# Kernel tuning notes

Hardware: AMD Instinct MI355X
Metric: run time of the kernel (lower is better)

The kernel has to match this reference:

```python
import jax, jax.numpy as jnp
import numpy as np

N, P, C = 100000, 64, 128
DIST_TH = 0.1


def setup_inputs() -> dict:
    key = jax.random.key(0)
    ks = jax.random.split(key, 12)
    xyz = jax.random.uniform(ks[0], (N, 3), jnp.float32) * 10.0  # room coords in [0,10)^3
    feature = jax.random.normal(ks[1], (N, C), jnp.float32)
    center = jax.random.uniform(ks[2], (P, 3), jnp.float32) * 10.0
    normal = jax.random.normal(ks[3], (P, 3), jnp.float32)
    normal = normal / jnp.linalg.norm(normal, axis=1, keepdims=True)
    pmin = center - 1.5  # axis-aligned extent used on axes 0,1
    pmax = center + 1.5
    inp = {
        'feature': feature, 'xyz': xyz,
        'plane_center': center, 'plane_normal': normal,
        'plane_min': pmin, 'plane_max': pmax,
        'W1': jax.random.normal(ks[4], (C, 2 * C), jnp.float32) * (1.0 / np.sqrt(C)),
        's1': jnp.ones((2 * C,), jnp.float32), 'b1': jnp.zeros((2 * C,), jnp.float32),
        'W2': jax.random.normal(ks[5], (2 * C, C), jnp.float32) * (1.0 / np.sqrt(2 * C)),
        's2': jnp.ones((C,), jnp.float32), 'b2': jnp.zeros((C,), jnp.float32),
        'W3': jax.random.normal(ks[6], (C, 1), jnp.float32) * (1.0 / np.sqrt(C)),
        'b3': jnp.zeros((1,), jnp.float32),
        'Wa': jax.random.normal(ks[7], (C, C), jnp.float32) * (1.0 / np.sqrt(C)),
        'Wm': jax.random.normal(ks[8], (C, C), jnp.float32) * (1.0 / np.sqrt(C)),
        'bm': jnp.zeros((C,), jnp.float32),
    }
    return inp


def reference(feature, xyz, plane_center, plane_normal, plane_min, plane_max,
              W1, s1, b1, W2, s2, b2, W3, b3, Wa, Wm, bm):
    # pointwise MLP (shared across planes): fc1 (conv+BN+ReLU), fc2 (conv+BN+ReLU)
    h = jax.nn.relu((feature @ W1) * s1 + b1)          # [N, 2C]
    h2 = jax.nn.relu((h @ W2) * s2 + b2)               # [N, C] == plane_feature
    logit = (h2 @ W3 + b3)[:, 0]                        # [N] fc3 logits (plane_result)

    # per-plane point membership masks (dense [N, P])
    proj = xyz @ plane_normal.T                         # [N, P]
    offs = jnp.sum(plane_center * plane_normal, axis=1) # [P]
    dist_mask = jnp.abs(proj - offs[None, :]) < DIST_TH
    rng = ((xyz[:, None, 0] >= plane_min[None, :, 0]) & (xyz[:, None, 0] < plane_max[None, :, 0]) &
           (xyz[:, None, 1] >= plane_min[None, :, 1]) & (xyz[:, None, 1] < plane_max[None, :, 1]))
    mask = dist_mask & rng                              # [N, P]

    on_sel = jax.nn.sigmoid(logit) > 0.5                # [N]
    on_mask = (mask & on_sel[:, None]).astype(feature.dtype)
    off_mask = (mask & ~on_sel[:, None]).astype(feature.dtype)

    # attention pooling: masked softmax over points, per plane, per channel
    a = h2 @ Wa                                         # [N, C] att activations
    e = jnp.exp(a - jnp.max(a, axis=0, keepdims=True))  # stable exp, [N, C]
    eh = e * h2

    def att_pool(m):                                    # m: [N, P] float
        num = jnp.einsum('np,nc->pc', m, eh)
        den = jnp.einsum('np,nc->pc', m, e)
        agg = num / (den + 1e-9)                        # masked-softmax weighted sum
        return jax.nn.relu(agg @ Wm + bm)               # att_pooling.mlp (conv+ReLU)

    ori = jnp.concatenate([plane_center, plane_normal, plane_min, plane_max], axis=1)  # [P, 12]
    on_feat = jnp.concatenate([att_pool(on_mask), ori], axis=1)    # [P, C+12]
    off_feat = jnp.concatenate([att_pool(off_mask), ori], axis=1)  # [P, C+12]
    return logit, on_feat, off_feat
```

## Files before the change

kernel.cpp:

```cpp
#include <hip/hip_runtime.h>

#define NPTS 100000
#define P 64
#define C 128
#define CHUNKS 16
#define CHUNK_PTS 6250
#define CHUNK_PAD 6400

typedef __bf16 bf16_t;
typedef __bf16 bf16x8 __attribute__((ext_vector_type(8)));
typedef float floatx4 __attribute__((ext_vector_type(4)));


__global__ __launch_bounds__(256) void prep_kernel(
    const float* __restrict__ W1, const float* __restrict__ s1,
    const float* __restrict__ W2, const float* __restrict__ s2,
    const float* __restrict__ Wa,
    bf16_t* __restrict__ W1t, bf16_t* __restrict__ W2t, bf16_t* __restrict__ Wat)
{
  int i0 = blockIdx.x * blockDim.x + threadIdx.x;
  int stride = gridDim.x * blockDim.x;
  for (int i = i0; i < 256 * 128; i += stride) {
    int n = i >> 7, k = i & 127;
    W1t[i] = (bf16_t)(W1[k * 256 + n] * s1[n]);
  }
  for (int i = i0; i < 128 * 256; i += stride) {
    int n = i >> 8, k = i & 255;
    W2t[i] = (bf16_t)(W2[k * 128 + n] * s2[n]);
  }
  for (int i = i0; i < 128 * 128; i += stride) {
    int n = i >> 7, k = i & 127;
    Wat[i] = (bf16_t)(Wa[k * 128 + n]);
  }
}

__global__ __launch_bounds__(256) void main_kernel(
    const float* __restrict__ feature,
    const float* __restrict__ b1, const float* __restrict__ b2,
    const float* __restrict__ W3, const float* __restrict__ b3,
    const bf16_t* __restrict__ W1t, const bf16_t* __restrict__ W2t,
    const bf16_t* __restrict__ Wat,
    bf16_t* __restrict__ rec, float* __restrict__ out_logit)
{
  __shared__ __align__(16) char smem[17408 + 33792 + 512];
  bf16_t* A1  = (bf16_t*)smem;
  bf16_t* Hs  = (bf16_t*)(smem + 17408);
  bf16_t* aB  = (bf16_t*)(smem + 17408);
  float*  w3S = (float*)(smem + 17408 + 33792);

  const int tid  = threadIdx.x;
  const int wave = tid >> 6, lane = tid & 63;
  const int quad = lane >> 4, l16 = lane & 15;
  const int m0 = blockIdx.x * 64;

  if (tid < 128) w3S[tid] = W3[tid];

  for (int i = tid; i < 64 * 32; i += 256) {
    int r = i >> 5, c4 = i & 31;
    float4 v = make_float4(0.f, 0.f, 0.f, 0.f);
    if (m0 + r < NPTS) v = *(const float4*)(feature + (size_t)(m0 + r) * C + c4 * 4);
    bf16_t* dst = A1 + r * 136 + c4 * 4;
    dst[0] = (bf16_t)v.x; dst[1] = (bf16_t)v.y; dst[2] = (bf16_t)v.z; dst[3] = (bf16_t)v.w;
  }
  __syncthreads();

  const floatx4 zero4 = {0.f, 0.f, 0.f, 0.f};

  {
    floatx4 acc[4][4];
#pragma unroll
    for (int mt = 0; mt < 4; ++mt)
#pragma unroll
      for (int nt = 0; nt < 4; ++nt) acc[mt][nt] = zero4;
#pragma unroll
    for (int kt = 0; kt < 4; ++kt) {
      bf16x8 af[4], bf[4];
#pragma unroll
      for (int mt = 0; mt < 4; ++mt)
        af[mt] = *(const bf16x8*)(A1 + (mt * 16 + l16) * 136 + kt * 32 + quad * 8);
#pragma unroll
      for (int nt = 0; nt < 4; ++nt)
        bf[nt] = *(const bf16x8*)(W1t + (wave * 64 + nt * 16 + l16) * 128 + kt * 32 + quad * 8);
#pragma unroll
      for (int mt = 0; mt < 4; ++mt)
#pragma unroll
        for (int nt = 0; nt < 4; ++nt)
          acc[mt][nt] = __builtin_amdgcn_mfma_f32_16x16x32_bf16(af[mt], bf[nt], acc[mt][nt], 0, 0, 0);
    }
#pragma unroll
    for (int nt = 0; nt < 4; ++nt) {
      int col = wave * 64 + nt * 16 + l16;
      float bias = b1[col];
#pragma unroll
      for (int mt = 0; mt < 4; ++mt)
#pragma unroll
        for (int r = 0; r < 4; ++r) {
          float hv = fmaxf(acc[mt][nt][r] + bias, 0.f);
          Hs[(mt * 16 + quad * 4 + r) * 264 + col] = (bf16_t)hv;
        }
    }
  }
  __syncthreads();

  {
    floatx4 acc[4][2];
#pragma unroll
    for (int mt = 0; mt < 4; ++mt) { acc[mt][0] = zero4; acc[mt][1] = zero4; }
#pragma unroll
    for (int kt = 0; kt < 8; ++kt) {
      bf16x8 af[4], bf[2];
#pragma unroll
      for (int mt = 0; mt < 4; ++mt)
        af[mt] = *(const bf16x8*)(Hs + (mt * 16 + l16) * 264 + kt * 32 + quad * 8);
#pragma unroll
      for (int nt = 0; nt < 2; ++nt)
        bf[nt] = *(const bf16x8*)(W2t + (wave * 32 + nt * 16 + l16) * 256 + kt * 32 + quad * 8);
#pragma unroll
      for (int mt = 0; mt < 4; ++mt)
#pragma unroll
        for (int nt = 0; nt < 2; ++nt)
          acc[mt][nt] = __builtin_amdgcn_mfma_f32_16x16x32_bf16(af[mt], bf[nt], acc[mt][nt], 0, 0, 0);
    }
#pragma unroll
    for (int nt = 0; nt < 2; ++nt) {
      int col = wave * 32 + nt * 16 + l16;
      float bias = b2[col];
#pragma unroll
      for (int mt = 0; mt < 4; ++mt)
#pragma unroll
        for (int r = 0; r < 4; ++r) {
          float hv = fmaxf(acc[mt][nt][r] + bias, 0.f);
          A1[(mt * 16 + quad * 4 + r) * 136 + col] = (bf16_t)hv;
        }
    }
  }
  __syncthreads();

  {
    floatx4 acc[4][2];
#pragma unroll
    for (int mt = 0; mt < 4; ++mt) { acc[mt][0] = zero4; acc[mt][1] = zero4; }
#pragma unroll
    for (int kt = 0; kt < 4; ++kt) {
      bf16x8 af[4], bf[2];
#pragma unroll
      for (int mt = 0; mt < 4; ++mt)
        af[mt] = *(const bf16x8*)(A1 + (mt * 16 + l16) * 136 + kt * 32 + quad * 8);
#pragma unroll
      for (int nt = 0; nt < 2; ++nt)
        bf[nt] = *(const bf16x8*)(Wat + (wave * 32 + nt * 16 + l16) * 128 + kt * 32 + quad * 8);
#pragma unroll
      for (int mt = 0; mt < 4; ++mt)
#pragma unroll
        for (int nt = 0; nt < 2; ++nt)
          acc[mt][nt] = __builtin_amdgcn_mfma_f32_16x16x32_bf16(af[mt], bf[nt], acc[mt][nt], 0, 0, 0);
    }
#pragma unroll
    for (int nt = 0; nt < 2; ++nt) {
      int col = wave * 32 + nt * 16 + l16;
#pragma unroll
      for (int mt = 0; mt < 4; ++mt)
#pragma unroll
        for (int r = 0; r < 4; ++r)
          aB[(mt * 16 + quad * 4 + r) * 136 + col] = (bf16_t)acc[mt][nt][r];
    }
  }
  __syncthreads();

  {
    const int m = tid >> 2, g = tid & 3, c0g = g * 32;
    const int mg = m0 + m;
    float lsum = 0.f;
#pragma unroll 8
    for (int c = 0; c < 32; ++c)
      lsum += (float)A1[m * 136 + c0g + c] * w3S[c0g + c];
    lsum += __shfl_xor(lsum, 1);
    lsum += __shfl_xor(lsum, 2);
    if (mg < NPTS && g == 0) out_logit[mg] = lsum + b3[0];
  }

  for (int i = tid; i < 64 * 64; i += 256) {
    int pt = i >> 6, slot = i & 63;
    if (m0 + pt < NPTS) {
      const bf16_t* src = (slot < 32) ? (aB + pt * 136 + slot * 4)
                                      : (A1 + pt * 136 + (slot - 32) * 4);
      uint2 v = *(const uint2*)src;
      *(uint2*)(rec + (size_t)(m0 + pt) * 256 + slot * 4) = v;
    }
  }
}

__global__ __launch_bounds__(256) void pool_kernel(
    const float* __restrict__ xyz, const float* __restrict__ out_logit,
    const bf16_t* __restrict__ rec,
    const float* __restrict__ ctr, const float* __restrict__ nrm,
    const float* __restrict__ pmn, const float* __restrict__ pmx,
    float* __restrict__ partial)
{
  const int plane = blockIdx.x >> 4;
  const int chunk = blockIdx.x & 15;
  const int tid = threadIdx.x, lane = tid & 63;

  __shared__ float accS[4][128];
  for (int i = tid; i < 512; i += 256) ((float*)accS)[i] = 0.f;

  const float nx = nrm[plane * 3], ny = nrm[plane * 3 + 1], nz = nrm[plane * 3 + 2];
  const float offs = ctr[plane * 3] * nx + ctr[plane * 3 + 1] * ny + ctr[plane * 3 + 2] * nz;
  const float mnx = pmn[plane * 3], mny = pmn[plane * 3 + 1];
  const float mxx = pmx[plane * 3], mxy = pmx[plane * 3 + 1];
  __syncthreads();

  const int base = chunk * CHUNK_PTS;
  float nOn0 = 0, nOn1 = 0, dOn0 = 0, dOn1 = 0;
  float nOf0 = 0, nOf1 = 0, dOf0 = 0, dOf1 = 0;

  for (int i = tid; i < CHUNK_PAD; i += 256) {
    int pt = base + i;
    bool hit = false;
    if (i < CHUNK_PTS) {
      float x = xyz[pt * 3], y = xyz[pt * 3 + 1], z = xyz[pt * 3 + 2];
      float proj = x * nx + y * ny + z * nz;
      hit = (fabsf(proj - offs) < 0.1f) &&
            (x >= mnx) && (x < mxx) && (y >= mny) && (y < mxy);
    }
    unsigned long long m = __ballot(hit);
    while (m) {
      int l = __builtin_ctzll(m);
      m &= m - 1;
      int hpt = __shfl(pt, l);
      float lg = out_logit[hpt];
      const unsigned* r32 = (const unsigned*)(rec + (size_t)hpt * 256);
      unsigned ap = r32[lane];
      unsigned hp = r32[64 + lane];
      float a0 = __uint_as_float(ap << 16);
      float a1 = __uint_as_float(ap & 0xffff0000u);
      float h0 = __uint_as_float(hp << 16);
      float h1 = __uint_as_float(hp & 0xffff0000u);
      float e0 = __expf(a0), e1 = __expf(a1);
      if (lg > 0.f) { nOn0 += e0 * h0; nOn1 += e1 * h1; dOn0 += e0; dOn1 += e1; }
      else          { nOf0 += e0 * h0; nOf1 += e1 * h1; dOf0 += e0; dOf1 += e1; }
    }
  }

  atomicAdd(&accS[0][lane * 2],     nOn0);
  atomicAdd(&accS[0][lane * 2 + 1], nOn1);
  atomicAdd(&accS[1][lane * 2],     dOn0);
  atomicAdd(&accS[1][lane * 2 + 1], dOn1);
  atomicAdd(&accS[2][lane * 2],     nOf0);
  atomicAdd(&accS[2][lane * 2 + 1], nOf1);
  atomicAdd(&accS[3][lane * 2],     dOf0);
  atomicAdd(&accS[3][lane * 2 + 1], dOf1);
  __syncthreads();

  float* dst = partial + (size_t)blockIdx.x * 512;
  for (int i = tid; i < 512; i += 256) dst[i] = ((float*)accS)[i];
}

__global__ __launch_bounds__(128) void finalize_kernel(
    const float* __restrict__ partial,
    const float* __restrict__ Wm, const float* __restrict__ bm,
    const float* __restrict__ ctr, const float* __restrict__ nrm,
    const float* __restrict__ pmn, const float* __restrict__ pmx,
    float* __restrict__ out)
{
  int sel = blockIdx.x >> 6, p = blockIdx.x & 63;
  int j = threadIdx.x;
  float num = 0.f, den = 0.f;
  const float* bp = partial + (size_t)p * 16 * 512 + sel * 2 * 128;
#pragma unroll
  for (int k = 0; k < 16; ++k) {
    num += bp[k * 512 + j];
    den += bp[k * 512 + 128 + j];
  }
  __shared__ float aggS[128];
  aggS[j] = num / (den + 1e-9f);
  __syncthreads();
  float s = bm[j];
#pragma unroll 4
  for (int c = 0; c < C; ++c) s += aggS[c] * Wm[c * C + j];
  s = fmaxf(s, 0.f);
  float* dst = out + NPTS + sel * (P * 140) + p * 140;
  dst[j] = s;
  if (j < 12) {
    float v;
    if (j < 3)      v = ctr[p * 3 + j];
    else if (j < 6) v = nrm[p * 3 + j - 3];
    else if (j < 9) v = pmn[p * 3 + j - 6];
    else            v = pmx[p * 3 + j - 9];
    dst[C + j] = v;
  }
}

extern "C" void kernel_launch(void* const* d_in, const int* in_sizes, int n_in,
                              void* d_out, int out_size, void* d_ws, size_t ws_size,
                              hipStream_t stream)
{
  const float* feature = (const float*)d_in[0];
  const float* xyz     = (const float*)d_in[1];
  const float* ctr     = (const float*)d_in[2];
  const float* nrm     = (const float*)d_in[3];
  const float* pmn     = (const float*)d_in[4];
  const float* pmx     = (const float*)d_in[5];
  const float* W1      = (const float*)d_in[6];
  const float* s1      = (const float*)d_in[7];
  const float* b1      = (const float*)d_in[8];
  const float* W2      = (const float*)d_in[9];
  const float* s2      = (const float*)d_in[10];
  const float* b2      = (const float*)d_in[11];
  const float* W3      = (const float*)d_in[12];
  const float* b3      = (const float*)d_in[13];
  const float* Wa      = (const float*)d_in[14];
  const float* Wm      = (const float*)d_in[15];
  const float* bm      = (const float*)d_in[16];
  float* out = (float*)d_out;

  char* ws = (char*)d_ws;
  bf16_t* W1t = (bf16_t*)(ws);
  bf16_t* W2t = (bf16_t*)(ws + 65536);
  bf16_t* Wat = (bf16_t*)(ws + 131072);
  bf16_t* rec = (bf16_t*)(ws + 163840);
  float* partial = (float*)(ws + 163840 + (size_t)NPTS * 512);

  prep_kernel<<<64, 256, 0, stream>>>(W1, s1, W2, s2, Wa, W1t, W2t, Wat);
  main_kernel<<<(NPTS + 63) / 64, 256, 0, stream>>>(
      feature, b1, b2, W3, b3, W1t, W2t, Wat, rec, out);
  pool_kernel<<<64 * CHUNKS, 256, 0, stream>>>(
      xyz, out, rec, ctr, nrm, pmn, pmx, partial);
  finalize_kernel<<<128, 128, 0, stream>>>(partial, Wm, bm, ctr, nrm, pmn, pmx, out);
}
```

Baseline: 194.5 us.

## Process two point tiles per block with prefetch of next tile's features

Each main_kernel block now handles 128 points as two 64-point tiles. The second tile's feature rows are loaded into registers before the first tile is computed, so global load latency overlaps the MFMA work. Biases are cached in shared memory, the bf16 conversion stores and the logit dot product are vectorized, and the finalize kernel splits its partial reduction and Wm matvec across 256 threads. The cost is half as many blocks and higher register pressure from the 8 prefetched float4s, which may lower occupancy.

Result: no change. 196.9 us (+1.3%).

```diff
diff --git a/kernel.cpp b/kernel.cpp
--- a/kernel.cpp
+++ b/kernel.cpp
@@ -8,6 +8,7 @@
 #define CHUNK_PAD 6400
 
 typedef __bf16 bf16_t;
+typedef __bf16 bf16x4 __attribute__((ext_vector_type(4)));
 typedef __bf16 bf16x8 __attribute__((ext_vector_type(8)));
 typedef float floatx4 __attribute__((ext_vector_type(4)));
 
@@ -31,6 +32,144 @@
   for (int i = i0; i < 128 * 128; i += stride) {
     int n = i >> 7, k = i & 127;
     Wat[i] = (bf16_t)(Wa[k * 128 + n]);
+  }
+}
+
+__device__ __forceinline__ void process_tile(
+    bf16_t* A1, bf16_t* Hs, bf16_t* aB,
+    const float* w3S, const float* b1S, const float* b2S, float b3v,
+    const bf16_t* __restrict__ W1t, const bf16_t* __restrict__ W2t,
+    const bf16_t* __restrict__ Wat,
+    bf16_t* __restrict__ rec, float* __restrict__ out_logit,
+    int m0, int tid, int wave, int lane, int quad, int l16)
+{
+  const floatx4 zero4 = {0.f, 0.f, 0.f, 0.f};
+
+  {
+    floatx4 acc[4][4];
+#pragma unroll
+    for (int mt = 0; mt < 4; ++mt)
+#pragma unroll
+      for (int nt = 0; nt < 4; ++nt) acc[mt][nt] = zero4;
+#pragma unroll
+    for (int kt = 0; kt < 4; ++kt) {
+      bf16x8 af[4], bf[4];
+#pragma unroll
+      for (int mt = 0; mt < 4; ++mt)
+        af[mt] = *(const bf16x8*)(A1 + (mt * 16 + l16) * 136 + kt * 32 + quad * 8);
+#pragma unroll
+      for (int nt = 0; nt < 4; ++nt)
+        bf[nt] = *(const bf16x8*)(W1t + (wave * 64 + nt * 16 + l16) * 128 + kt * 32 + quad * 8);
+#pragma unroll
+      for (int mt = 0; mt < 4; ++mt)
+#pragma unroll
+        for (int nt = 0; nt < 4; ++nt)
+          acc[mt][nt] = __builtin_amdgcn_mfma_f32_16x16x32_bf16(af[mt], bf[nt], acc[mt][nt], 0, 0, 0);
+    }
+#pragma unroll
+    for (int nt = 0; nt < 4; ++nt) {
+      int col = wave * 64 + nt * 16 + l16;
+      float bias = b1S[col];
+#pragma unroll
+      for (int mt = 0; mt < 4; ++mt)
+#pragma unroll
+        for (int r = 0; r < 4; ++r) {
+          float hv = fmaxf(acc[mt][nt][r] + bias, 0.f);
+          Hs[(mt * 16 + quad * 4 + r) * 264 + col] = (bf16_t)hv;
+        }
+    }
+  }
+  __syncthreads();
+
+  {
+    floatx4 acc[4][2];
+#pragma unroll
+    for (int mt = 0; mt < 4; ++mt) { acc[mt][0] = zero4; acc[mt][1] = zero4; }
+#pragma unroll
+    for (int kt = 0; kt < 8; ++kt) {
+      bf16x8 af[4], bf[2];
+#pragma unroll
+      for (int mt = 0; mt < 4; ++mt)
+        af[mt] = *(const bf16x8*)(Hs + (mt * 16 + l16) * 264 + kt * 32 + quad * 8);
+#pragma unroll
+      for (int nt = 0; nt < 2; ++nt)
+        bf[nt] = *(const bf16x8*)(W2t + (wave * 32 + nt * 16 + l16) * 256 + kt * 32 + quad * 8);
+#pragma unroll
+      for (int mt = 0; mt < 4; ++mt)
+#pragma unroll
+        for (int nt = 0; nt < 2; ++nt)
+          acc[mt][nt] = __builtin_amdgcn_mfma_f32_16x16x32_bf16(af[mt], bf[nt], acc[mt][nt], 0, 0, 0);
+    }
+#pragma unroll
+    for (int nt = 0; nt < 2; ++nt) {
+      int col = wave * 32 + nt * 16 + l16;
+      float bias = b2S[col];
+#pragma unroll
+      for (int mt = 0; mt < 4; ++mt)
+#pragma unroll
+        for (int r = 0; r < 4; ++r) {
+          float hv = fmaxf(acc[mt][nt][r] + bias, 0.f);
+          A1[(mt * 16 + quad * 4 + r) * 136 + col] = (bf16_t)hv;
+        }
+    }
+  }
+  __syncthreads();
+
+  {
+    floatx4 acc[4][2];
+#pragma unroll
+    for (int mt = 0; mt < 4; ++mt) { acc[mt][0] = zero4; acc[mt][1] = zero4; }
+#pragma unroll
+    for (int kt = 0; kt < 4; ++kt) {
+      bf16x8 af[4], bf[2];
+#pragma unroll
+      for (int mt = 0; mt < 4; ++mt)
+        af[mt] = *(const bf16x8*)(A1 + (mt * 16 + l16) * 136 + kt * 32 + quad * 8);
+#pragma unroll
+      for (int nt = 0; nt < 2; ++nt)
+        bf[nt] = *(const bf16x8*)(Wat + (wave * 32 + nt * 16 + l16) * 128 + kt * 32 + quad * 8);
+#pragma unroll
+      for (int mt = 0; mt < 4; ++mt)
+#pragma unroll
+        for (int nt = 0; nt < 2; ++nt)
+          acc[mt][nt] = __builtin_amdgcn_mfma_f32_16x16x32_bf16(af[mt], bf[nt], acc[mt][nt], 0, 0, 0);
+    }
+#pragma unroll
+    for (int nt = 0; nt < 2; ++nt) {
+      int col = wave * 32 + nt * 16 + l16;
+#pragma unroll
+      for (int mt = 0; mt < 4; ++mt)
+#pragma unroll
+        for (int r = 0; r < 4; ++r)
+          aB[(mt * 16 + quad * 4 + r) * 136 + col] = (bf16_t)acc[mt][nt][r];
+    }
+  }
+  __syncthreads();
+
+  {
+    const int m = tid >> 2, g = tid & 3, c0g = g * 32;
+    const int mg = m0 + m;
+    float lsum = 0.f;
+#pragma unroll
+    for (int cc = 0; cc < 4; ++cc) {
+      bf16x8 v = *(const bf16x8*)(A1 + m * 136 + c0g + cc * 8);
+#pragma unroll
+      for (int j = 0; j < 8; ++j)
+        lsum += (float)v[j] * w3S[c0g + cc * 8 + j];
+    }
+    lsum += __shfl_xor(lsum, 1);
+    lsum += __shfl_xor(lsum, 2);
+    if (mg < NPTS && g == 0) out_logit[mg] = lsum + b3v;
+  }
+
+  for (int i = tid; i < 64 * 64; i += 256) {
+    int pt = i >> 6, slot = i & 63;
+    if (m0 + pt < NPTS) {
+      const bf16_t* src = (slot < 32) ? (aB + pt * 136 + slot * 4)
+                                      : (A1 + pt * 136 + (slot - 32) * 4);
+      uint2 v = *(const uint2*)src;
+      *(uint2*)(rec + (size_t)(m0 + pt) * 256 + slot * 4) = v;
+    }
   }
 }
 
@@ -42,152 +181,59 @@
     const bf16_t* __restrict__ Wat,
     bf16_t* __restrict__ rec, float* __restrict__ out_logit)
 {
-  __shared__ __align__(16) char smem[17408 + 33792 + 512];
+  __shared__ __align__(16) char smem[17408 + 33792 + 512 + 1024 + 512];
   bf16_t* A1  = (bf16_t*)smem;
   bf16_t* Hs  = (bf16_t*)(smem + 17408);
   bf16_t* aB  = (bf16_t*)(smem + 17408);
   float*  w3S = (float*)(smem + 17408 + 33792);
+  float*  b1S = (float*)(smem + 17408 + 33792 + 512);
+  float*  b2S = (float*)(smem + 17408 + 33792 + 512 + 1024);
 
   const int tid  = threadIdx.x;
   const int wave = tid >> 6, lane = tid & 63;
   const int quad = lane >> 4, l16 = lane & 15;
-  const int m0 = blockIdx.x * 64;
+  const int m0 = blockIdx.x * 128;
 
   if (tid < 128) w3S[tid] = W3[tid];
-
-  for (int i = tid; i < 64 * 32; i += 256) {
-    int r = i >> 5, c4 = i & 31;
+  if (tid < 128) b2S[tid] = b2[tid];
+  b1S[tid] = b1[tid];
+  const float b3v = b3[0];
+
+  const int r0 = tid >> 5, c4 = tid & 31;
+
+#pragma unroll
+  for (int j = 0; j < 8; ++j) {
+    int r = r0 + j * 8;
     float4 v = make_float4(0.f, 0.f, 0.f, 0.f);
     if (m0 + r < NPTS) v = *(const float4*)(feature + (size_t)(m0 + r) * C + c4 * 4);
-    bf16_t* dst = A1 + r * 136 + c4 * 4;
-    dst[0] = (bf16_t)v.x; dst[1] = (bf16_t)v.y; dst[2] = (bf16_t)v.z; dst[3] = (bf16_t)v.w;
-  }
-  __syncthreads();
-
-  const floatx4 zero4 = {0.f, 0.f, 0.f, 0.f};
-
-  {
-    floatx4 acc[4][4];
-#pragma unroll
-    for (int mt = 0; mt < 4; ++mt)
-#pragma unroll
-      for (int nt = 0; nt < 4; ++nt) acc[mt][nt] = zero4;
-#pragma unroll
-    for (int kt = 0; kt < 4; ++kt) {
-      bf16x8 af[4], bf[4];
-#pragma unroll
-      for (int mt = 0; mt < 4; ++mt)
-        af[mt] = *(const bf16x8*)(A1 + (mt * 16 + l16) * 136 + kt * 32 + quad * 8);
-#pragma unroll
-      for (int nt = 0; nt < 4; ++nt)
-        bf[nt] = *(const bf16x8*)(W1t + (wave * 64 + nt * 16 + l16) * 128 + kt * 32 + quad * 8);
-#pragma unroll
-      for (int mt = 0; mt < 4; ++mt)
-#pragma unroll
-        for (int nt = 0; nt < 4; ++nt)
-          acc[mt][nt] = __builtin_amdgcn_mfma_f32_16x16x32_bf16(af[mt], bf[nt], acc[mt][nt], 0, 0, 0);
-    }
-#pragma unroll
-    for (int nt = 0; nt < 4; ++nt) {
-      int col = wave * 64 + nt * 16 + l16;
-      float bias = b1[col];
-#pragma unroll
-      for (int mt = 0; mt < 4; ++mt)
-#pragma unroll
-        for (int r = 0; r < 4; ++r) {
-          float hv = fmaxf(acc[mt][nt][r] + bias, 0.f);
-          Hs[(mt * 16 + quad * 4 + r) * 264 + col] = (bf16_t)hv;
-        }
-    }
-  }
-  __syncthreads();
-
-  {
-    floatx4 acc[4][2];
-#pragma unroll
-    for (int mt = 0; mt < 4; ++mt) { acc[mt][0] = zero4; acc[mt][1] = zero4; }
-#pragma unroll
-    for (int kt = 0; kt < 8; ++kt) {
-      bf16x8 af[4], bf[2];
-#pragma unroll
-      for (int mt = 0; mt < 4; ++mt)
-        af[mt] = *(const bf16x8*)(Hs + (mt * 16 + l16) * 264 + kt * 32 + quad * 8);
-#pragma unroll
-      for (int nt = 0; nt < 2; ++nt)
-        bf[nt] = *(const bf16x8*)(W2t + (wave * 32 + nt * 16 + l16) * 256 + kt * 32 + quad * 8);
-#pragma unroll
-      for (int mt = 0; mt < 4; ++mt)
-#pragma unroll
-        for (int nt = 0; nt < 2; ++nt)
-          acc[mt][nt] = __builtin_amdgcn_mfma_f32_16x16x32_bf16(af[mt], bf[nt], acc[mt][nt], 0, 0, 0);
-    }
-#pragma unroll
-    for (int nt = 0; nt < 2; ++nt) {
-      int col = wave * 32 + nt * 16 + l16;
-      float bias = b2[col];
-#pragma unroll
-      for (int mt = 0; mt < 4; ++mt)
-#pragma unroll
-        for (int r = 0; r < 4; ++r) {
-          float hv = fmaxf(acc[mt][nt][r] + bias, 0.f);
-          A1[(mt * 16 + quad * 4 + r) * 136 + col] = (bf16_t)hv;
-        }
-    }
-  }
-  __syncthreads();
-
-  {
-    floatx4 acc[4][2];
-#pragma unroll
-    for (int mt = 0; mt < 4; ++mt) { acc[mt][0] = zero4; acc[mt][1] = zero4; }
-#pragma unroll
-    for (int kt = 0; kt < 4; ++kt) {
-      bf16x8 af[4], bf[2];
-#pragma unroll
-      for (int mt = 0; mt < 4; ++mt)
-        af[mt] = *(const bf16x8*)(A1 + (mt * 16 + l16) * 136 + kt * 32 + quad * 8);
-#pragma unroll
-      for (int nt = 0; nt < 2; ++nt)
-        bf[nt] = *(const bf16x8*)(Wat + (wave * 32 + nt * 16 + l16) * 128 + kt * 32 + quad * 8);
-#pragma unroll
-      for (int mt = 0; mt < 4; ++mt)
-#pragma unroll
-        for (int nt = 0; nt < 2; ++nt)
-          acc[mt][nt] = __builtin_amdgcn_mfma_f32_16x16x32_bf16(af[mt], bf[nt], acc[mt][nt], 0, 0, 0);
-    }
-#pragma unroll
-    for (int nt = 0; nt < 2; ++nt) {
-      int col = wave * 32 + nt * 16 + l16;
-#pragma unroll
-      for (int mt = 0; mt < 4; ++mt)
-#pragma unroll
-        for (int r = 0; r < 4; ++r)
-          aB[(mt * 16 + quad * 4 + r) * 136 + col] = (bf16_t)acc[mt][nt][r];
-    }
-  }
-  __syncthreads();
-
-  {
-    const int m = tid >> 2, g = tid & 3, c0g = g * 32;
-    const int mg = m0 + m;
-    float lsum = 0.f;
-#pragma unroll 8
-    for (int c = 0; c < 32; ++c)
-      lsum += (float)A1[m * 136 + c0g + c] * w3S[c0g + c];
-    lsum += __shfl_xor(lsum, 1);
-    lsum += __shfl_xor(lsum, 2);
-    if (mg < NPTS && g == 0) out_logit[mg] = lsum + b3[0];
-  }
-
-  for (int i = tid; i < 64 * 64; i += 256) {
-    int pt = i >> 6, slot = i & 63;
-    if (m0 + pt < NPTS) {
-      const bf16_t* src = (slot < 32) ? (aB + pt * 136 + slot * 4)
-                                      : (A1 + pt * 136 + (slot - 32) * 4);
-      uint2 v = *(const uint2*)src;
-      *(uint2*)(rec + (size_t)(m0 + pt) * 256 + slot * 4) = v;
-    }
-  }
+    bf16x4 o = {(bf16_t)v.x, (bf16_t)v.y, (bf16_t)v.z, (bf16_t)v.w};
+    *(bf16x4*)(A1 + r * 136 + c4 * 4) = o;
+  }
+  __syncthreads();
+
+  float4 f2[8];
+#pragma unroll
+  for (int j = 0; j < 8; ++j) {
+    int r = r0 + j * 8;
+    f2[j] = make_float4(0.f, 0.f, 0.f, 0.f);
+    if (m0 + 64 + r < NPTS)
+      f2[j] = *(const float4*)(feature + (size_t)(m0 + 64 + r) * C + c4 * 4);
+  }
+
+  process_tile(A1, Hs, aB, w3S, b1S, b2S, b3v, W1t, W2t, Wat, rec, out_logit,
+               m0, tid, wave, lane, quad, l16);
+  __syncthreads();
+
+#pragma unroll
+  for (int j = 0; j < 8; ++j) {
+    int r = r0 + j * 8;
+    bf16x4 o = {(bf16_t)f2[j].x, (bf16_t)f2[j].y, (bf16_t)f2[j].z, (bf16_t)f2[j].w};
+    *(bf16x4*)(A1 + r * 136 + c4 * 4) = o;
+  }
+  __syncthreads();
+
+  process_tile(A1, Hs, aB, w3S, b1S, b2S, b3v, W1t, W2t, Wat, rec, out_logit,
+               m0 + 64, tid, wave, lane, quad, l16);
 }
 
 __global__ __launch_bounds__(256) void pool_kernel(
@@ -256,7 +302,7 @@
   for (int i = tid; i < 512; i += 256) dst[i] = ((float*)accS)[i];
 }
 
-__global__ __launch_bounds__(128) void finalize_kernel(
+__global__ __launch_bounds__(256) void finalize_kernel(
     const float* __restrict__ partial,
     const float* __restrict__ Wm, const float* __restrict__ bm,
     const float* __restrict__ ctr, const float* __restrict__ nrm,
@@ -264,30 +310,41 @@
     float* __restrict__ out)
 {
   int sel = blockIdx.x >> 6, p = blockIdx.x & 63;
-  int j = threadIdx.x;
+  int tid = threadIdx.x, j = tid & 127, half = tid >> 7;
+  __shared__ float numS[2][128], denS[2][128], aggS[128], sumS[2][128];
+
+  const float* bp = partial + ((size_t)p * 16 + half * 8) * 512 + sel * 256;
   float num = 0.f, den = 0.f;
-  const float* bp = partial + (size_t)p * 16 * 512 + sel * 2 * 128;
-#pragma unroll
-  for (int k = 0; k < 16; ++k) {
+#pragma unroll
+  for (int k = 0; k < 8; ++k) {
     num += bp[k * 512 + j];
     den += bp[k * 512 + 128 + j];
   }
-  __shared__ float aggS[128];
-  aggS[j] = num / (den + 1e-9f);
-  __syncthreads();
-  float s = bm[j];
-#pragma unroll 4
-  for (int c = 0; c < C; ++c) s += aggS[c] * Wm[c * C + j];
-  s = fmaxf(s, 0.f);
+  numS[half][j] = num;
+  denS[half][j] = den;
+  __syncthreads();
+  if (tid < 128)
+    aggS[tid] = (numS[0][tid] + numS[1][tid]) / (denS[0][tid] + denS[1][tid] + 1e-9f);
+  __syncthreads();
+
+  float s = 0.f;
+  const int cbase = half * 64;
+#pragma unroll 8
+  for (int c = 0; c < 64; ++c)
+    s += aggS[cbase + c] * Wm[(cbase + c) * C + j];
+  sumS[half][j] = s;
+  __syncthreads();
+
   float* dst = out + NPTS + sel * (P * 140) + p * 140;
-  dst[j] = s;
-  if (j < 12) {
+  if (tid < 128)
+    dst[tid] = fmaxf(sumS[0][tid] + sumS[1][tid] + bm[tid], 0.f);
+  if (tid < 12) {
     float v;
-    if (j < 3)      v = ctr[p * 3 + j];
-    else if (j < 6) v = nrm[p * 3 + j - 3];
-    else if (j < 9) v = pmn[p * 3 + j - 6];
-    else            v = pmx[p * 3 + j - 9];
-    dst[C + j] = v;
+    if (tid < 3)      v = ctr[p * 3 + tid];
+    else if (tid < 6) v = nrm[p * 3 + tid - 3];
+    else if (tid < 9) v = pmn[p * 3 + tid - 6];
+    else              v = pmx[p * 3 + tid - 9];
+    dst[C + tid] = v;
   }
 }
 
@@ -322,9 +379,9 @@
   float* partial = (float*)(ws + 163840 + (size_t)NPTS * 512);
 
   prep_kernel<<<64, 256, 0, stream>>>(W1, s1, W2, s2, Wa, W1t, W2t, Wat);
-  main_kernel<<<(NPTS + 63) / 64, 256, 0, stream>>>(
+  main_kernel<<<(NPTS + 127) / 128, 256, 0, stream>>>(
       feature, b1, b2, W3, b3, W1t, W2t, Wat, rec, out);
   pool_kernel<<<64 * CHUNKS, 256, 0, stream>>>(
       xyz, out, rec, ctr, nrm, pmn, pmx, partial);
-  finalize_kernel<<<128, 128, 0, stream>>>(partial, Wm, bm, ctr, nrm, pmn, pmx, out);
-}
+  finalize_kernel<<<128, 256, 0, stream>>>(partial, Wm, bm, ctr, nrm, pmn, pmx, out);
+}
```
